# Kernel optimization log

Hardware: AMD Instinct MI355X
Metric: run time of the kernel (lower is better)

## Reference

```python
import jax, jax.numpy as jnp
import numpy as np

B, L = 512, 256
N_NEG, L_NEG = 20, 64
VOCAB = 50000  # table has VOCAB+1 rows (row 0 = padding)
D = 100
K = 14
LAMBDA = 1.0


def setup_inputs() -> dict:
    key = jax.random.key(0)
    k1, k2, k3, k4, k5, k6, k7, k8 = jax.random.split(key, 8)
    pos_ids = jax.random.randint(k1, (B, L), 0, VOCAB + 1)
    neg_ids = jax.random.randint(k2, (B, N_NEG, L_NEG), 0, VOCAB + 1)
    emb_table = jax.random.normal(k3, (VOCAB + 1, D), dtype=jnp.float32) * 0.1
    emb_table = emb_table.at[0].set(0.0)  # padding row is zeros
    W_att = jax.random.normal(k4, (D, D), dtype=jnp.float32) * 0.05
    Wk = jax.random.normal(k5, (D, K), dtype=jnp.float32) * 0.1
    bk = jnp.zeros((K,), dtype=jnp.float32)
    Wf = jax.random.normal(k6, (K, D), dtype=jnp.float32) * 0.1  # aspect matrix (kmeans-init in original)
    bf = jnp.zeros((D,), dtype=jnp.float32)
    return {"pos_ids": pos_ids, "neg_ids": neg_ids, "emb_table": emb_table,
            "W_att": W_att, "Wk": Wk, "bk": bk, "Wf": Wf, "bf": bf}


def reference(pos_ids, neg_ids, emb_table, W_att, Wk, bk, Wf, bf):
    mask = pos_ids != 0                                   # [B, L]
    maskf = mask.astype(jnp.float32)
    e = emb_table[pos_ids]                                # [B, L, D]
    # --- masked aspect attention ---
    ys = jnp.mean(e, axis=-2)                             # [B, D] (unmasked mean, as in source)
    eW = jnp.einsum('bld,de->ble', e, W_att) * maskf[..., None]
    f = jnp.einsum('bld,bd->bl', eW, ys)[..., None]       # [B, L, 1]
    f = f + ((~mask).astype(f.dtype) * -1e9)[..., None]
    att = jax.nn.softmax(f, axis=-2)                      # softmax over L
    zs = jnp.sum(att * e, axis=-2)                        # [B, D]
    # --- aspect probabilities and reconstruction ---
    pt = jax.nn.sigmoid(zs @ Wk + bk)                     # [B, K]
    rs = pt @ Wf + bf                                     # [B, D]
    # --- orthogonality reg (faithful to source: uses the NORMS, normalize(...)[1]) ---
    norms = jnp.linalg.norm(Wf, axis=1, keepdims=True)    # [K, 1]
    reg = norms @ norms.T - jnp.ones((K, K), dtype=jnp.float32)
    reg = jnp.sqrt(jnp.sum(reg * reg))                    # Frobenius norm
    # --- margin loss ---
    pos_term = jnp.sum(rs * zs)                           # tensordot(rs, zs, [[0,1],[0,1]])
    a = jnp.mean(emb_table[neg_ids], axis=-2)             # [B, N_NEG, D]
    # tensordot(a, expand_dims(rs,-2), [[0,2],[0,2]]) -> [N_NEG, 1], then reduce_sum
    neg_term = jnp.sum(jnp.einsum('bnd,bd->n', a, rs))
    loss = jax.nn.relu(1.0 - neg_term + pos_term) + LAMBDA * reg
    return (loss, pt, rs)
```

## Files before the change

### kernel.cpp

```cpp
#include <hip/hip_runtime.h>
#include <hip/hip_bf16.h>

#if !__has_builtin(__builtin_amdgcn_cvt_pk_f32_fp8) || !__has_builtin(__builtin_amdgcn_cvt_pk_fp8_f32)
#include <hip/hip_fp8.h>
#endif

#define Bx 512
#define Lx 256
#define Dx 100
#define Kx 14
#define VROWS 50001
#define NEG_ROWS 1280
#define TPB 512
#define NGRP 16

#define PAD8  128
#define RAW8  100

typedef float floatx2 __attribute__((ext_vector_type(2)));

__device__ __forceinline__ float dot4(float4 a, float4 b) {
    return a.x * b.x + a.y * b.y + a.z * b.z + a.w * b.w;
}

__device__ __forceinline__ float4 fp8x4_dec(unsigned u) {
#if __has_builtin(__builtin_amdgcn_cvt_pk_f32_fp8)
    floatx2 lo = __builtin_amdgcn_cvt_pk_f32_fp8((int)u, false);
    floatx2 hi = __builtin_amdgcn_cvt_pk_f32_fp8((int)u, true);
    return make_float4(lo.x, lo.y, hi.x, hi.y);
#else
    __hip_fp8_e4m3 a, b, c, d;
    a.__x = (unsigned char)(u & 0xFF);
    b.__x = (unsigned char)((u >> 8) & 0xFF);
    c.__x = (unsigned char)((u >> 16) & 0xFF);
    d.__x = (unsigned char)((u >> 24) & 0xFF);
    return make_float4((float)a, (float)b, (float)c, (float)d);
#endif
}

__device__ __forceinline__ unsigned fp8x4_enc(float4 v) {
#if __has_builtin(__builtin_amdgcn_cvt_pk_fp8_f32)
    int p = 0;
    p = __builtin_amdgcn_cvt_pk_fp8_f32(v.x, v.y, p, false);
    p = __builtin_amdgcn_cvt_pk_fp8_f32(v.z, v.w, p, true);
    return (unsigned)p;
#else
    __hip_fp8_e4m3 a(v.x), b(v.y), c(v.z), d(v.w);
    return (unsigned)a.__x | ((unsigned)b.__x << 8) |
           ((unsigned)c.__x << 16) | ((unsigned)d.__x << 24);
#endif
}

__global__ __launch_bounds__(256) void convert_kernel(
    const float* __restrict__ table, unsigned char* __restrict__ tb8,
    const float* __restrict__ Wf, float* __restrict__ acc, int RS8, int padded)
{
    const int tid = threadIdx.x;
    const int gid = blockIdx.x * 256 + tid;
    if (gid < 4) acc[gid] = 0.0f;

    const int row = gid >> 5;
    const int c   = gid & 31;
    if (row < VROWS) {
        if (c < 25) {
            const float4 v = *reinterpret_cast<const float4*>(
                table + (size_t)row * Dx + c * 4);
            *reinterpret_cast<unsigned*>(tb8 + (size_t)row * RS8 + c * 4) = fp8x4_enc(v);
        } else if (padded) {
            *reinterpret_cast<unsigned*>(tb8 + (size_t)row * RS8 + c * 4) = 0u;
        }
    }

    if (blockIdx.x == 0) {
        __shared__ float n_sh[Kx];
        __shared__ float r_sh[256];
        if (tid < Kx) {
            const float4* w4 = reinterpret_cast<const float4*>(Wf + (size_t)tid * Dx);
            float s = 0.f;
            #pragma unroll
            for (int i = 0; i < 25; ++i) { const float4 w = w4[i]; s += dot4(w, w); }
            n_sh[tid] = sqrtf(s);
        }
        __syncthreads();
        float vv = 0.f;
        if (tid < Kx * Kx) {
            const int i = tid / Kx;
            const int j = tid - i * Kx;
            const float x = n_sh[i] * n_sh[j] - 1.0f;
            vv = x * x;
        }
        r_sh[tid] = vv;
        __syncthreads();
        for (int s = 128; s > 0; s >>= 1) {
            if (tid < s) r_sh[tid] += r_sh[tid + s];
            __syncthreads();
        }
        if (tid == 0) acc[3] = sqrtf(r_sh[0]);
    }
}

__global__ __launch_bounds__(TPB) void fused_all(
    const int* __restrict__ pos_ids, const int* __restrict__ neg_ids,
    const unsigned char* __restrict__ tb8,
    const float* __restrict__ W_att, const float* __restrict__ Wk,
    const float* __restrict__ bk, const float* __restrict__ Wf,
    const float* __restrict__ bf, float* __restrict__ pt_out,
    float* __restrict__ rs_out, float* __restrict__ acc,
    float* __restrict__ out, int RS8)
{
    const int tid  = threadIdx.x;
    const int grp  = tid >> 5;
    const int lane = tid & 31;
    const int b    = blockIdx.x;

    __shared__ __align__(16) unsigned rowbuf[Lx][26];
    __shared__ int   ids[Lx];
    __shared__ int   idn[NEG_ROWS];
    __shared__ __align__(16) float4 part4[NGRP][26];
    __shared__ __align__(16) float ys_sh[104];
    __shared__ __align__(16) float t_sh[104];
    __shared__ float zs_sh[104];
    __shared__ float pt_sh[Kx];
    __shared__ float m_sh[NGRP], s_sh[NGRP], sc_sh[NGRP];
    __shared__ float wred[8][2];

    float* pf = (float*)part4;

    if (tid < Lx) ids[tid] = pos_ids[(size_t)b * Lx + tid] * RS8;
    for (int i = tid; i < NEG_ROWS; i += TPB)
        idn[i] = neg_ids[(size_t)b * NEG_ROWS + i] * RS8;
    __syncthreads();

    float4 na = {0.f, 0.f, 0.f, 0.f};
    if (lane < 25) {
        const int o = lane * 4;
        float4 a0 = {0,0,0,0}, a1 = {0,0,0,0}, a2 = {0,0,0,0}, a3 = {0,0,0,0};
        for (int r = grp; r < NEG_ROWS; r += 64) {
            const float4 v0 = fp8x4_dec(*(const unsigned*)(tb8 + (size_t)idn[r]      + o));
            const float4 v1 = fp8x4_dec(*(const unsigned*)(tb8 + (size_t)idn[r + 16] + o));
            const float4 v2 = fp8x4_dec(*(const unsigned*)(tb8 + (size_t)idn[r + 32] + o));
            const float4 v3 = fp8x4_dec(*(const unsigned*)(tb8 + (size_t)idn[r + 48] + o));
            a0.x += v0.x; a0.y += v0.y; a0.z += v0.z; a0.w += v0.w;
            a1.x += v1.x; a1.y += v1.y; a1.z += v1.z; a1.w += v1.w;
            a2.x += v2.x; a2.y += v2.y; a2.z += v2.z; a2.w += v2.w;
            a3.x += v3.x; a3.y += v3.y; a3.z += v3.z; a3.w += v3.w;
        }
        na.x = a0.x + a1.x + a2.x + a3.x;
        na.y = a0.y + a1.y + a2.y + a3.y;
        na.z = a0.z + a1.z + a2.z + a3.z;
        na.w = a0.w + a1.w + a2.w + a3.w;
    }

    if (lane < 25) {
        const int o = lane * 4;
        float4 a0 = {0,0,0,0}, a1 = {0,0,0,0}, a2 = {0,0,0,0}, a3 = {0,0,0,0};
        for (int r = grp; r < Lx; r += 64) {
            const unsigned u0 = *(const unsigned*)(tb8 + (size_t)ids[r]      + o);
            const unsigned u1 = *(const unsigned*)(tb8 + (size_t)ids[r + 16] + o);
            const unsigned u2 = *(const unsigned*)(tb8 + (size_t)ids[r + 32] + o);
            const unsigned u3 = *(const unsigned*)(tb8 + (size_t)ids[r + 48] + o);
            rowbuf[r][lane]      = u0;
            rowbuf[r + 16][lane] = u1;
            rowbuf[r + 32][lane] = u2;
            rowbuf[r + 48][lane] = u3;
            const float4 v0 = fp8x4_dec(u0);
            const float4 v1 = fp8x4_dec(u1);
            const float4 v2 = fp8x4_dec(u2);
            const float4 v3 = fp8x4_dec(u3);
            a0.x += v0.x; a0.y += v0.y; a0.z += v0.z; a0.w += v0.w;
            a1.x += v1.x; a1.y += v1.y; a1.z += v1.z; a1.w += v1.w;
            a2.x += v2.x; a2.y += v2.y; a2.z += v2.z; a2.w += v2.w;
            a3.x += v3.x; a3.y += v3.y; a3.z += v3.z; a3.w += v3.w;
        }
        a0.x += a1.x + a2.x + a3.x; a0.y += a1.y + a2.y + a3.y;
        a0.z += a1.z + a2.z + a3.z; a0.w += a1.w + a2.w + a3.w;
        part4[grp][lane] = a0;
    }
    __syncthreads();
    if (tid < Dx) {
        float s = 0.f;
        #pragma unroll
        for (int g = 0; g < NGRP; ++g) s += pf[g * 104 + tid];
        ys_sh[tid] = s * (1.0f / Lx);
    }
    __syncthreads();

    if (tid < Dx) {
        const float4* w4 = reinterpret_cast<const float4*>(W_att + (size_t)tid * Dx);
        const float4* y4 = reinterpret_cast<const float4*>(ys_sh);
        float s = 0.f;
        #pragma unroll
        for (int i = 0; i < 25; ++i) s += dot4(w4[i], y4[i]);
        t_sh[tid] = s;
    }
    __syncthreads();

    {
        const float4 tl = (lane < 25) ? ((const float4*)t_sh)[lane]
                                      : make_float4(0.f, 0.f, 0.f, 0.f);
        float m = -1e30f, ssum = 0.f;
        float4 za = {0.f, 0.f, 0.f, 0.f};
        for (int r = grp; r < Lx; r += 32) {
            const int id0 = ids[r];
            const int id1 = ids[r + 16];
            float4 e0 = {0,0,0,0}, e1 = {0,0,0,0};
            if (lane < 25) {
                e0 = fp8x4_dec(rowbuf[r][lane]);
                e1 = fp8x4_dec(rowbuf[r + 16][lane]);
            }
            float d0 = dot4(e0, tl);
            float d1 = dot4(e1, tl);
            #pragma unroll
            for (int o = 16; o > 0; o >>= 1) {
                d0 += __shfl_xor(d0, o, 32);
                d1 += __shfl_xor(d1, o, 32);
            }
            const float f0 = (id0 != 0) ? d0 : -1e30f;
            const float f1 = (id1 != 0) ? d1 : -1e30f;
            const float mn = fmaxf(m, fmaxf(f0, f1));
            const float sc = expf(m - mn);
            const float w0 = (id0 != 0) ? expf(d0 - mn) : 0.f;
            const float w1 = (id1 != 0) ? expf(d1 - mn) : 0.f;
            ssum = ssum * sc + w0 + w1;
            za.x = za.x * sc + w0 * e0.x + w1 * e1.x;
            za.y = za.y * sc + w0 * e0.y + w1 * e1.y;
            za.z = za.z * sc + w0 * e0.z + w1 * e1.z;
            za.w = za.w * sc + w0 * e0.w + w1 * e1.w;
            m = mn;
        }
        if (lane == 0) { m_sh[grp] = m; s_sh[grp] = ssum; }
        if (lane < 25) part4[grp][lane] = za;
    }
    __syncthreads();
    if (tid < NGRP) {
        float M = -1e30f;
        #pragma unroll
        for (int g = 0; g < NGRP; ++g) M = fmaxf(M, m_sh[g]);
        sc_sh[tid] = expf(m_sh[tid] - M);
    }
    __syncthreads();
    if (tid < Dx) {
        float S = 0.f, z = 0.f;
        #pragma unroll
        for (int g = 0; g < NGRP; ++g) {
            S += s_sh[g] * sc_sh[g];
            z += pf[g * 104 + tid] * sc_sh[g];
        }
        zs_sh[tid] = z / S;
    }
    __syncthreads();

    if (tid < Kx) {
        float s = bk[tid];
        for (int d = 0; d < Dx; ++d) s += zs_sh[d] * Wk[d * Kx + tid];
        const float pk = 1.0f / (1.0f + expf(-s));
        pt_sh[tid] = pk;
        pt_out[(size_t)b * Kx + tid] = pk;
    }
    __syncthreads();

    float posc = 0.f, negc = 0.f, rs_reg = 0.f;
    if (tid < Dx) {
        float r = bf[tid];
        #pragma unroll
        for (int k = 0; k < Kx; ++k) r += pt_sh[k] * Wf[k * Dx + tid];
        rs_out[(size_t)b * Dx + tid] = r;
        rs_reg = r;
        posc = r * zs_sh[tid];
    }

    if (lane < 25) part4[grp][lane] = na;
    __syncthreads();
    if (tid < Dx) {
        float gsum = 0.f;
        #pragma unroll
        for (int g = 0; g < NGRP; ++g) gsum += pf[g * 104 + tid];
        negc = gsum * rs_reg;
    }

    #pragma unroll
    for (int o = 32; o > 0; o >>= 1) {
        posc += __shfl_xor(posc, o);
        negc += __shfl_xor(negc, o);
    }
    const int wid = tid >> 6;
    if ((tid & 63) == 0) { wred[wid][0] = posc; wred[wid][1] = negc; }
    __syncthreads();

    if (tid == 0) {
        float P = 0.f, N = 0.f;
        #pragma unroll
        for (int w = 0; w < 8; ++w) { P += wred[w][0]; N += wred[w][1]; }
        atomicAdd(&acc[0], P);
        atomicAdd(&acc[1], N);
        __threadfence();
        const unsigned t = atomicAdd(reinterpret_cast<unsigned int*>(acc) + 2, 1u);
        if (t == (unsigned)(Bx - 1)) {
            const float pos = atomicAdd(&acc[0], 0.0f);
            const float neg = atomicAdd(&acc[1], 0.0f);
            const float reg = atomicAdd(&acc[3], 0.0f);
            const float margin = 1.0f - neg * (1.0f / 64.0f) + pos;
            out[0] = fmaxf(margin, 0.0f) + reg;
        }
    }
}

extern "C" void kernel_launch(void* const* d_in, const int* in_sizes, int n_in,
                              void* d_out, int out_size, void* d_ws, size_t ws_size,
                              hipStream_t stream) {
    const int*   pos_ids = (const int*)  d_in[0];
    const int*   neg_ids = (const int*)  d_in[1];
    const float* table   = (const float*)d_in[2];
    const float* W_att   = (const float*)d_in[3];
    const float* Wk      = (const float*)d_in[4];
    const float* bk      = (const float*)d_in[5];
    const float* Wf      = (const float*)d_in[6];
    const float* bf      = (const float*)d_in[7];

    float* out    = (float*)d_out;
    float* pt_out = out + 1;
    float* rs_out = out + 1 + (size_t)Bx * Kx;

    const size_t need_pad = (size_t)VROWS * PAD8 + 16 + 4 * sizeof(float);
    const int padded = (ws_size >= need_pad) ? 1 : 0;
    const int RS8 = padded ? PAD8 : RAW8;

    unsigned char* tb8 = (unsigned char*)d_ws;
    size_t acc_off = (size_t)VROWS * RS8;
    acc_off = (acc_off + 15) & ~(size_t)15;
    float* acc = (float*)((char*)d_ws + acc_off);

    const int nthreads = VROWS * 32;
    convert_kernel<<<(nthreads + 255) / 256, 256, 0, stream>>>(
        table, tb8, Wf, acc, RS8, padded);
    fused_all<<<Bx, TPB, 0, stream>>>(
        pos_ids, neg_ids, tb8, W_att, Wk, bk, Wf, bf,
        pt_out, rs_out, acc, out, RS8);
}
```

Before: 128.6 us.

## Gather padded fp8 rows with 16-byte loads and fold partial sums via shuffles

Adds a specialised kernel for the 128-byte padded fp8 table layout. Each lane gathers 16 bytes per row with uint4 loads, so 8 lanes cover a row and four rows are in flight per group. Partial sums are reduced with cross-lane shuffles before being written to shared memory. The aim is fewer, wider gather instructions in place of many 4-byte loads. Exp calls also switch to __expf, and the unpadded path is kept as a fallback kernel.

Result: faster. 125.9 us, median of 2 (-2.1%).

```diff
diff --git a/kernel.cpp b/kernel.cpp
--- a/kernel.cpp
+++ b/kernel.cpp
@@ -51,6 +51,34 @@
 #endif
 }
 
+__device__ __forceinline__ void acc16(uint4 u, float4* A) {
+    const float4 v0 = fp8x4_dec(u.x);
+    const float4 v1 = fp8x4_dec(u.y);
+    const float4 v2 = fp8x4_dec(u.z);
+    const float4 v3 = fp8x4_dec(u.w);
+    A[0].x += v0.x; A[0].y += v0.y; A[0].z += v0.z; A[0].w += v0.w;
+    A[1].x += v1.x; A[1].y += v1.y; A[1].z += v1.z; A[1].w += v1.w;
+    A[2].x += v2.x; A[2].y += v2.y; A[2].z += v2.z; A[2].w += v2.w;
+    A[3].x += v3.x; A[3].y += v3.y; A[3].z += v3.z; A[3].w += v3.w;
+}
+
+__device__ __forceinline__ void fold4(float4* A) {
+    #pragma unroll
+    for (int k = 0; k < 4; ++k) {
+        A[k].x += __shfl_xor(A[k].x, 8);
+        A[k].y += __shfl_xor(A[k].y, 8);
+        A[k].z += __shfl_xor(A[k].z, 8);
+        A[k].w += __shfl_xor(A[k].w, 8);
+    }
+    #pragma unroll
+    for (int k = 0; k < 4; ++k) {
+        A[k].x += __shfl_xor(A[k].x, 16);
+        A[k].y += __shfl_xor(A[k].y, 16);
+        A[k].z += __shfl_xor(A[k].z, 16);
+        A[k].w += __shfl_xor(A[k].w, 16);
+    }
+}
+
 __global__ __launch_bounds__(256) void convert_kernel(
     const float* __restrict__ table, unsigned char* __restrict__ tb8,
     const float* __restrict__ Wf, float* __restrict__ acc, int RS8, int padded)
@@ -99,24 +127,24 @@
     }
 }
 
-__global__ __launch_bounds__(TPB) void fused_all(
+__global__ __launch_bounds__(TPB) void fused_all_pad(
     const int* __restrict__ pos_ids, const int* __restrict__ neg_ids,
     const unsigned char* __restrict__ tb8,
     const float* __restrict__ W_att, const float* __restrict__ Wk,
     const float* __restrict__ bk, const float* __restrict__ Wf,
     const float* __restrict__ bf, float* __restrict__ pt_out,
     float* __restrict__ rs_out, float* __restrict__ acc,
-    float* __restrict__ out, int RS8)
+    float* __restrict__ out)
 {
     const int tid  = threadIdx.x;
     const int grp  = tid >> 5;
     const int lane = tid & 31;
     const int b    = blockIdx.x;
 
-    __shared__ __align__(16) unsigned rowbuf[Lx][26];
+    __shared__ __align__(16) unsigned rowbuf[Lx][32];
     __shared__ int   ids[Lx];
     __shared__ int   idn[NEG_ROWS];
-    __shared__ __align__(16) float4 part4[NGRP][26];
+    __shared__ __align__(16) float pf2[NGRP][128];
     __shared__ __align__(16) float ys_sh[104];
     __shared__ __align__(16) float t_sh[104];
     __shared__ float zs_sh[104];
@@ -124,63 +152,51 @@
     __shared__ float m_sh[NGRP], s_sh[NGRP], sc_sh[NGRP];
     __shared__ float wred[8][2];
 
-    float* pf = (float*)part4;
-
-    if (tid < Lx) ids[tid] = pos_ids[(size_t)b * Lx + tid] * RS8;
+    if (tid < Lx) ids[tid] = pos_ids[(size_t)b * Lx + tid] << 7;
     for (int i = tid; i < NEG_ROWS; i += TPB)
-        idn[i] = neg_ids[(size_t)b * NEG_ROWS + i] * RS8;
-    __syncthreads();
-
-    float4 na = {0.f, 0.f, 0.f, 0.f};
-    if (lane < 25) {
-        const int o = lane * 4;
-        float4 a0 = {0,0,0,0}, a1 = {0,0,0,0}, a2 = {0,0,0,0}, a3 = {0,0,0,0};
-        for (int r = grp; r < NEG_ROWS; r += 64) {
-            const float4 v0 = fp8x4_dec(*(const unsigned*)(tb8 + (size_t)idn[r]      + o));
-            const float4 v1 = fp8x4_dec(*(const unsigned*)(tb8 + (size_t)idn[r + 16] + o));
-            const float4 v2 = fp8x4_dec(*(const unsigned*)(tb8 + (size_t)idn[r + 32] + o));
-            const float4 v3 = fp8x4_dec(*(const unsigned*)(tb8 + (size_t)idn[r + 48] + o));
-            a0.x += v0.x; a0.y += v0.y; a0.z += v0.z; a0.w += v0.w;
-            a1.x += v1.x; a1.y += v1.y; a1.z += v1.z; a1.w += v1.w;
-            a2.x += v2.x; a2.y += v2.y; a2.z += v2.z; a2.w += v2.w;
-            a3.x += v3.x; a3.y += v3.y; a3.z += v3.z; a3.w += v3.w;
-        }
-        na.x = a0.x + a1.x + a2.x + a3.x;
-        na.y = a0.y + a1.y + a2.y + a3.y;
-        na.z = a0.z + a1.z + a2.z + a3.z;
-        na.w = a0.w + a1.w + a2.w + a3.w;
-    }
-
-    if (lane < 25) {
-        const int o = lane * 4;
-        float4 a0 = {0,0,0,0}, a1 = {0,0,0,0}, a2 = {0,0,0,0}, a3 = {0,0,0,0};
-        for (int r = grp; r < Lx; r += 64) {
-            const unsigned u0 = *(const unsigned*)(tb8 + (size_t)ids[r]      + o);
-            const unsigned u1 = *(const unsigned*)(tb8 + (size_t)ids[r + 16] + o);
-            const unsigned u2 = *(const unsigned*)(tb8 + (size_t)ids[r + 32] + o);
-            const unsigned u3 = *(const unsigned*)(tb8 + (size_t)ids[r + 48] + o);
-            rowbuf[r][lane]      = u0;
-            rowbuf[r + 16][lane] = u1;
-            rowbuf[r + 32][lane] = u2;
-            rowbuf[r + 48][lane] = u3;
-            const float4 v0 = fp8x4_dec(u0);
-            const float4 v1 = fp8x4_dec(u1);
-            const float4 v2 = fp8x4_dec(u2);
-            const float4 v3 = fp8x4_dec(u3);
-            a0.x += v0.x; a0.y += v0.y; a0.z += v0.z; a0.w += v0.w;
-            a1.x += v1.x; a1.y += v1.y; a1.z += v1.z; a1.w += v1.w;
-            a2.x += v2.x; a2.y += v2.y; a2.z += v2.z; a2.w += v2.w;
-            a3.x += v3.x; a3.y += v3.y; a3.z += v3.z; a3.w += v3.w;
-        }
-        a0.x += a1.x + a2.x + a3.x; a0.y += a1.y + a2.y + a3.y;
-        a0.z += a1.z + a2.z + a3.z; a0.w += a1.w + a2.w + a3.w;
-        part4[grp][lane] = a0;
+        idn[i] = neg_ids[(size_t)b * NEG_ROWS + i] << 7;
+    __syncthreads();
+
+    const int j16  = (lane & 7) * 16;
+    const int j4   = (lane & 7) * 4;
+    const int rsub = lane >> 3;
+
+    float4 An[4] = {{0,0,0,0},{0,0,0,0},{0,0,0,0},{0,0,0,0}};
+    #pragma unroll 2
+    for (int it = 0; it < NEG_ROWS / 256; ++it) {
+        const int base = it * 256 + grp * 16 + rsub;
+        const uint4 u0 = *(const uint4*)(tb8 + (size_t)idn[base]      + j16);
+        const uint4 u1 = *(const uint4*)(tb8 + (size_t)idn[base + 4]  + j16);
+        const uint4 u2 = *(const uint4*)(tb8 + (size_t)idn[base + 8]  + j16);
+        const uint4 u3 = *(const uint4*)(tb8 + (size_t)idn[base + 12] + j16);
+        acc16(u0, An); acc16(u1, An); acc16(u2, An); acc16(u3, An);
+    }
+
+    {
+        const int base = grp * 16 + rsub;
+        const uint4 u0 = *(const uint4*)(tb8 + (size_t)ids[base]      + j16);
+        const uint4 u1 = *(const uint4*)(tb8 + (size_t)ids[base + 4]  + j16);
+        const uint4 u2 = *(const uint4*)(tb8 + (size_t)ids[base + 8]  + j16);
+        const uint4 u3 = *(const uint4*)(tb8 + (size_t)ids[base + 12] + j16);
+        *(uint4*)&rowbuf[base][j4]      = u0;
+        *(uint4*)&rowbuf[base + 4][j4]  = u1;
+        *(uint4*)&rowbuf[base + 8][j4]  = u2;
+        *(uint4*)&rowbuf[base + 12][j4] = u3;
+        float4 Ap[4] = {{0,0,0,0},{0,0,0,0},{0,0,0,0},{0,0,0,0}};
+        acc16(u0, Ap); acc16(u1, Ap); acc16(u2, Ap); acc16(u3, Ap);
+        fold4(Ap);
+        if (lane < 8) {
+            *(float4*)&pf2[grp][16 * lane]      = Ap[0];
+            *(float4*)&pf2[grp][16 * lane + 4]  = Ap[1];
+            *(float4*)&pf2[grp][16 * lane + 8]  = Ap[2];
+            *(float4*)&pf2[grp][16 * lane + 12] = Ap[3];
+        }
     }
     __syncthreads();
     if (tid < Dx) {
         float s = 0.f;
         #pragma unroll
-        for (int g = 0; g < NGRP; ++g) s += pf[g * 104 + tid];
+        for (int gg = 0; gg < NGRP; ++gg) s += pf2[gg][tid];
         ys_sh[tid] = s * (1.0f / Lx);
     }
     __syncthreads();
@@ -218,9 +234,9 @@
             const float f0 = (id0 != 0) ? d0 : -1e30f;
             const float f1 = (id1 != 0) ? d1 : -1e30f;
             const float mn = fmaxf(m, fmaxf(f0, f1));
-            const float sc = expf(m - mn);
-            const float w0 = (id0 != 0) ? expf(d0 - mn) : 0.f;
-            const float w1 = (id1 != 0) ? expf(d1 - mn) : 0.f;
+            const float sc = __expf(m - mn);
+            const float w0 = (id0 != 0) ? __expf(d0 - mn) : 0.f;
+            const float w1 = (id1 != 0) ? __expf(d1 - mn) : 0.f;
             ssum = ssum * sc + w0 + w1;
             za.x = za.x * sc + w0 * e0.x + w1 * e1.x;
             za.y = za.y * sc + w0 * e0.y + w1 * e1.y;
@@ -229,22 +245,22 @@
             m = mn;
         }
         if (lane == 0) { m_sh[grp] = m; s_sh[grp] = ssum; }
-        if (lane < 25) part4[grp][lane] = za;
+        if (lane < 25) ((float4*)pf2[grp])[lane] = za;
     }
     __syncthreads();
     if (tid < NGRP) {
         float M = -1e30f;
         #pragma unroll
-        for (int g = 0; g < NGRP; ++g) M = fmaxf(M, m_sh[g]);
-        sc_sh[tid] = expf(m_sh[tid] - M);
+        for (int gg = 0; gg < NGRP; ++gg) M = fmaxf(M, m_sh[gg]);
+        sc_sh[tid] = __expf(m_sh[tid] - M);
     }
     __syncthreads();
     if (tid < Dx) {
         float S = 0.f, z = 0.f;
         #pragma unroll
-        for (int g = 0; g < NGRP; ++g) {
-            S += s_sh[g] * sc_sh[g];
-            z += pf[g * 104 + tid] * sc_sh[g];
+        for (int gg = 0; gg < NGRP; ++gg) {
+            S += s_sh[gg] * sc_sh[gg];
+            z += pf2[gg][tid] * sc_sh[gg];
         }
         zs_sh[tid] = z / S;
     }
@@ -253,7 +269,7 @@
     if (tid < Kx) {
         float s = bk[tid];
         for (int d = 0; d < Dx; ++d) s += zs_sh[d] * Wk[d * Kx + tid];
-        const float pk = 1.0f / (1.0f + expf(-s));
+        const float pk = 1.0f / (1.0f + __expf(-s));
         pt_sh[tid] = pk;
         pt_out[(size_t)b * Kx + tid] = pk;
     }
@@ -269,12 +285,18 @@
         posc = r * zs_sh[tid];
     }
 
-    if (lane < 25) part4[grp][lane] = na;
+    fold4(An);
+    if (lane < 8) {
+        *(float4*)&pf2[grp][16 * lane]      = An[0];
+        *(float4*)&pf2[grp][16 * lane + 4]  = An[1];
+        *(float4*)&pf2[grp][16 * lane + 8]  = An[2];
+        *(float4*)&pf2[grp][16 * lane + 12] = An[3];
+    }
     __syncthreads();
     if (tid < Dx) {
         float gsum = 0.f;
         #pragma unroll
-        for (int g = 0; g < NGRP; ++g) gsum += pf[g * 104 + tid];
+        for (int gg = 0; gg < NGRP; ++gg) gsum += pf2[gg][tid];
         negc = gsum * rs_reg;
     }
 
@@ -305,6 +327,212 @@
     }
 }
 
+__global__ __launch_bounds__(TPB) void fused_all_compact(
+    const int* __restrict__ pos_ids, const int* __restrict__ neg_ids,
+    const unsigned char* __restrict__ tb8,
+    const float* __restrict__ W_att, const float* __restrict__ Wk,
+    const float* __restrict__ bk, const float* __restrict__ Wf,
+    const float* __restrict__ bf, float* __restrict__ pt_out,
+    float* __restrict__ rs_out, float* __restrict__ acc,
+    float* __restrict__ out, int RS8)
+{
+    const int tid  = threadIdx.x;
+    const int grp  = tid >> 5;
+    const int lane = tid & 31;
+    const int b    = blockIdx.x;
+
+    __shared__ __align__(16) unsigned rowbuf[Lx][26];
+    __shared__ int   ids[Lx];
+    __shared__ int   idn[NEG_ROWS];
+    __shared__ __align__(16) float4 part4[NGRP][26];
+    __shared__ __align__(16) float ys_sh[104];
+    __shared__ __align__(16) float t_sh[104];
+    __shared__ float zs_sh[104];
+    __shared__ float pt_sh[Kx];
+    __shared__ float m_sh[NGRP], s_sh[NGRP], sc_sh[NGRP];
+    __shared__ float wred[8][2];
+
+    float* pf = (float*)part4;
+
+    if (tid < Lx) ids[tid] = pos_ids[(size_t)b * Lx + tid] * RS8;
+    for (int i = tid; i < NEG_ROWS; i += TPB)
+        idn[i] = neg_ids[(size_t)b * NEG_ROWS + i] * RS8;
+    __syncthreads();
+
+    float4 na = {0.f, 0.f, 0.f, 0.f};
+    if (lane < 25) {
+        const int o = lane * 4;
+        float4 a0 = {0,0,0,0}, a1 = {0,0,0,0}, a2 = {0,0,0,0}, a3 = {0,0,0,0};
+        for (int r = grp; r < NEG_ROWS; r += 64) {
+            const float4 v0 = fp8x4_dec(*(const unsigned*)(tb8 + (size_t)idn[r]      + o));
+            const float4 v1 = fp8x4_dec(*(const unsigned*)(tb8 + (size_t)idn[r + 16] + o));
+            const float4 v2 = fp8x4_dec(*(const unsigned*)(tb8 + (size_t)idn[r + 32] + o));
+            const float4 v3 = fp8x4_dec(*(const unsigned*)(tb8 + (size_t)idn[r + 48] + o));
+            a0.x += v0.x; a0.y += v0.y; a0.z += v0.z; a0.w += v0.w;
+            a1.x += v1.x; a1.y += v1.y; a1.z += v1.z; a1.w += v1.w;
+            a2.x += v2.x; a2.y += v2.y; a2.z += v2.z; a2.w += v2.w;
+            a3.x += v3.x; a3.y += v3.y; a3.z += v3.z; a3.w += v3.w;
+        }
+        na.x = a0.x + a1.x + a2.x + a3.x;
+        na.y = a0.y + a1.y + a2.y + a3.y;
+        na.z = a0.z + a1.z + a2.z + a3.z;
+        na.w = a0.w + a1.w + a2.w + a3.w;
+    }
+
+    if (lane < 25) {
+        const int o = lane * 4;
+        float4 a0 = {0,0,0,0}, a1 = {0,0,0,0}, a2 = {0,0,0,0}, a3 = {0,0,0,0};
+        for (int r = grp; r < Lx; r += 64) {
+            const unsigned u0 = *(const unsigned*)(tb8 + (size_t)ids[r]      + o);
+            const unsigned u1 = *(const unsigned*)(tb8 + (size_t)ids[r + 16] + o);
+            const unsigned u2 = *(const unsigned*)(tb8 + (size_t)ids[r + 32] + o);
+            const unsigned u3 = *(const unsigned*)(tb8 + (size_t)ids[r + 48] + o);
+            rowbuf[r][lane]      = u0;
+            rowbuf[r + 16][lane] = u1;
+            rowbuf[r + 32][lane] = u2;
+            rowbuf[r + 48][lane] = u3;
+            const float4 v0 = fp8x4_dec(u0);
+            const float4 v1 = fp8x4_dec(u1);
+            const float4 v2 = fp8x4_dec(u2);
+            const float4 v3 = fp8x4_dec(u3);
+            a0.x += v0.x; a0.y += v0.y; a0.z += v0.z; a0.w += v0.w;
+            a1.x += v1.x; a1.y += v1.y; a1.z += v1.z; a1.w += v1.w;
+            a2.x += v2.x; a2.y += v2.y; a2.z += v2.z; a2.w += v2.w;
+            a3.x += v3.x; a3.y += v3.y; a3.z += v3.z; a3.w += v3.w;
+        }
+        a0.x += a1.x + a2.x + a3.x; a0.y += a1.y + a2.y + a3.y;
+        a0.z += a1.z + a2.z + a3.z; a0.w += a1.w + a2.w + a3.w;
+        part4[grp][lane] = a0;
+    }
+    __syncthreads();
+    if (tid < Dx) {
+        float s = 0.f;
+        #pragma unroll
+        for (int gg = 0; gg < NGRP; ++gg) s += pf[gg * 104 + tid];
+        ys_sh[tid] = s * (1.0f / Lx);
+    }
+    __syncthreads();
+
+    if (tid < Dx) {
+        const float4* w4 = reinterpret_cast<const float4*>(W_att + (size_t)tid * Dx);
+        const float4* y4 = reinterpret_cast<const float4*>(ys_sh);
+        float s = 0.f;
+        #pragma unroll
+        for (int i = 0; i < 25; ++i) s += dot4(w4[i], y4[i]);
+        t_sh[tid] = s;
+    }
+    __syncthreads();
+
+    {
+        const float4 tl = (lane < 25) ? ((const float4*)t_sh)[lane]
+                                      : make_float4(0.f, 0.f, 0.f, 0.f);
+        float m = -1e30f, ssum = 0.f;
+        float4 za = {0.f, 0.f, 0.f, 0.f};
+        for (int r = grp; r < Lx; r += 32) {
+            const int id0 = ids[r];
+            const int id1 = ids[r + 16];
+            float4 e0 = {0,0,0,0}, e1 = {0,0,0,0};
+            if (lane < 25) {
+                e0 = fp8x4_dec(rowbuf[r][lane]);
+                e1 = fp8x4_dec(rowbuf[r + 16][lane]);
+            }
+            float d0 = dot4(e0, tl);
+            float d1 = dot4(e1, tl);
+            #pragma unroll
+            for (int o = 16; o > 0; o >>= 1) {
+                d0 += __shfl_xor(d0, o, 32);
+                d1 += __shfl_xor(d1, o, 32);
+            }
+            const float f0 = (id0 != 0) ? d0 : -1e30f;
+            const float f1 = (id1 != 0) ? d1 : -1e30f;
+            const float mn = fmaxf(m, fmaxf(f0, f1));
+            const float sc = __expf(m - mn);
+            const float w0 = (id0 != 0) ? __expf(d0 - mn) : 0.f;
+            const float w1 = (id1 != 0) ? __expf(d1 - mn) : 0.f;
+            ssum = ssum * sc + w0 + w1;
+            za.x = za.x * sc + w0 * e0.x + w1 * e1.x;
+            za.y = za.y * sc + w0 * e0.y + w1 * e1.y;
+            za.z = za.z * sc + w0 * e0.z + w1 * e1.z;
+            za.w = za.w * sc + w0 * e0.w + w1 * e1.w;
+            m = mn;
+        }
+        if (lane == 0) { m_sh[grp] = m; s_sh[grp] = ssum; }
+        if (lane < 25) part4[grp][lane] = za;
+    }
+    __syncthreads();
+    if (tid < NGRP) {
+        float M = -1e30f;
+        #pragma unroll
+        for (int gg = 0; gg < NGRP; ++gg) M = fmaxf(M, m_sh[gg]);
+        sc_sh[tid] = __expf(m_sh[tid] - M);
+    }
+    __syncthreads();
+    if (tid < Dx) {
+        float S = 0.f, z = 0.f;
+        #pragma unroll
+        for (int gg = 0; gg < NGRP; ++gg) {
+            S += s_sh[gg] * sc_sh[gg];
+            z += pf[gg * 104 + tid] * sc_sh[gg];
+        }
+        zs_sh[tid] = z / S;
+    }
+    __syncthreads();
+
+    if (tid < Kx) {
+        float s = bk[tid];
+        for (int d = 0; d < Dx; ++d) s += zs_sh[d] * Wk[d * Kx + tid];
+        const float pk = 1.0f / (1.0f + __expf(-s));
+        pt_sh[tid] = pk;
+        pt_out[(size_t)b * Kx + tid] = pk;
+    }
+    __syncthreads();
+
+    float posc = 0.f, negc = 0.f, rs_reg = 0.f;
+    if (tid < Dx) {
+        float r = bf[tid];
+        #pragma unroll
+        for (int k = 0; k < Kx; ++k) r += pt_sh[k] * Wf[k * Dx + tid];
+        rs_out[(size_t)b * Dx + tid] = r;
+        rs_reg = r;
+        posc = r * zs_sh[tid];
+    }
+
+    if (lane < 25) part4[grp][lane] = na;
+    __syncthreads();
+    if (tid < Dx) {
+        float gsum = 0.f;
+        #pragma unroll
+        for (int gg = 0; gg < NGRP; ++gg) gsum += pf[gg * 104 + tid];
+        negc = gsum * rs_reg;
+    }
+
+    #pragma unroll
+    for (int o = 32; o > 0; o >>= 1) {
+        posc += __shfl_xor(posc, o);
+        negc += __shfl_xor(negc, o);
+    }
+    const int wid = tid >> 6;
+    if ((tid & 63) == 0) { wred[wid][0] = posc; wred[wid][1] = negc; }
+    __syncthreads();
+
+    if (tid == 0) {
+        float P = 0.f, N = 0.f;
+        #pragma unroll
+        for (int w = 0; w < 8; ++w) { P += wred[w][0]; N += wred[w][1]; }
+        atomicAdd(&acc[0], P);
+        atomicAdd(&acc[1], N);
+        __threadfence();
+        const unsigned t = atomicAdd(reinterpret_cast<unsigned int*>(acc) + 2, 1u);
+        if (t == (unsigned)(Bx - 1)) {
+            const float pos = atomicAdd(&acc[0], 0.0f);
+            const float neg = atomicAdd(&acc[1], 0.0f);
+            const float reg = atomicAdd(&acc[3], 0.0f);
+            const float margin = 1.0f - neg * (1.0f / 64.0f) + pos;
+            out[0] = fmaxf(margin, 0.0f) + reg;
+        }
+    }
+}
+
 extern "C" void kernel_launch(void* const* d_in, const int* in_sizes, int n_in,
                               void* d_out, int out_size, void* d_ws, size_t ws_size,
                               hipStream_t stream) {
@@ -333,7 +561,13 @@
     const int nthreads = VROWS * 32;
     convert_kernel<<<(nthreads + 255) / 256, 256, 0, stream>>>(
         table, tb8, Wf, acc, RS8, padded);
-    fused_all<<<Bx, TPB, 0, stream>>>(
-        pos_ids, neg_ids, tb8, W_att, Wk, bk, Wf, bf,
-        pt_out, rs_out, acc, out, RS8);
-}
+    if (padded) {
+        fused_all_pad<<<Bx, TPB, 0, stream>>>(
+            pos_ids, neg_ids, tb8, W_att, Wk, bk, Wf, bf,
+            pt_out, rs_out, acc, out);
+    } else {
+        fused_all_compact<<<Bx, TPB, 0, stream>>>(
+            pos_ids, neg_ids, tb8, W_att, Wk, bk, Wf, bf,
+            pt_out, rs_out, acc, out, RS8);
+    }
+}
```
